# Kernel tuning notes

Measured on AMD Instinct MI355X. Metric: run time of the kernel, lower is better.

## Reference

```python
import jax, jax.numpy as jnp
import numpy as np

N = 8192      # nodes
K_NN = 32     # kNN neighbors (module default k=32)
E = N * 16    # edges for TAGConv graph
EPS = 1e-5    # BatchNorm eps


def setup_inputs() -> dict:
    key = jax.random.key(0)
    ks = iter(jax.random.split(key, 64))
    def lin(i, o):
        return jax.random.normal(next(ks), (i, o), jnp.float32) / np.float32(np.sqrt(i))
    def vec(c, scale=0.02):
        return jax.random.normal(next(ks), (c,), jnp.float32) * scale
    inp = {}
    inp["pos"] = jax.random.normal(next(ks), (N, 3), jnp.float32)
    inp["x"] = jax.random.normal(next(ks), (N, 4), jnp.float32)
    inp["edge_index"] = jax.random.randint(next(ks), (2, E), 0, N, jnp.int32)
    # conv1 edge-MLP [2*3, 64, 64, 64]
    inp["mlp1_W1"] = lin(6, 64)
    inp["mlp1_W23"] = jnp.stack([lin(64, 64), lin(64, 64)])
    inp["mlp1_b"] = jnp.stack([vec(64) for _ in range(3)])
    inp["mlp1_g"] = 1.0 + jnp.stack([vec(64) for _ in range(3)])
    inp["mlp1_beta"] = jnp.stack([vec(64) for _ in range(3)])
    # conv2 edge-MLP [2*64, 128]
    inp["mlp2_W"] = lin(128, 128); inp["mlp2_b"] = vec(128)
    inp["mlp2_g"] = 1.0 + vec(128); inp["mlp2_beta"] = vec(128)
    # lin1 MLP [128+64, 512]
    inp["lin1_W"] = lin(192, 512); inp["lin1_b"] = vec(512)
    inp["lin1_g"] = 1.0 + vec(512); inp["lin1_beta"] = vec(512)
    # TAGConv(4,64,K=3) and TAGConv(64,128,K=3): K+1 hop weights each, shared bias
    inp["tag1_W"] = jnp.stack([lin(4, 64) for _ in range(4)]); inp["tag1_b"] = vec(64)
    inp["tag2_W"] = jnp.stack([lin(64, 128) for _ in range(4)]); inp["tag2_b"] = vec(128)
    # lin_gcnn1 MLP [128+64, 512]
    inp["lin2_W"] = lin(192, 512); inp["lin2_b"] = vec(512)
    inp["lin2_g"] = 1.0 + vec(512); inp["lin2_beta"] = vec(512)
    # mix_output: MLP[1024,512] -> Dropout -> MLP[512,256] -> Dropout -> Lin(256,1)
    inp["mix1_W"] = lin(1024, 512); inp["mix1_b"] = vec(512)
    inp["mix1_g"] = 1.0 + vec(512); inp["mix1_beta"] = vec(512)
    inp["mix2_W"] = lin(512, 256); inp["mix2_b"] = vec(256)
    inp["mix2_g"] = 1.0 + vec(256); inp["mix2_beta"] = vec(256)
    inp["out_W"] = lin(256, 1); inp["out_b"] = vec(1)
    return inp


def _bn_relu_lin(h, W, b, g, beta):
    # Seq(Linear, ReLU, BatchNorm1d) with training-mode (batch) statistics
    h = jax.nn.relu(h @ W + b)
    mu = jnp.mean(h, axis=0)
    var = jnp.var(h, axis=0)
    return g * (h - mu) * jax.lax.rsqrt(var + EPS) + beta


def _knn_idx(x, k):
    # brute-force kNN (loop=False: self excluded); indices are non-differentiable
    x = jax.lax.stop_gradient(x)
    sq = jnp.sum(x * x, axis=1)
    d = sq[:, None] + sq[None, :] - 2.0 * (x @ x.T)   # [N,N] squared dists
    n = x.shape[0]
    d = d.at[jnp.arange(n), jnp.arange(n)].set(jnp.inf)
    _, idx = jax.lax.top_k(-d, k)
    return idx                                        # [N,k]


def _edge_conv(x, k, mlp_fn):
    # DynamicEdgeConv: kNN graph on x, message MLP([x_i, x_j - x_i]), max-aggregate
    idx = _knn_idx(x, k)
    xj = x[idx]                                       # [N,k,C]
    xi = jnp.broadcast_to(x[:, None, :], xj.shape)
    e = jnp.concatenate([xi, xj - xi], axis=-1).reshape(-1, 2 * x.shape[1])
    h = mlp_fn(e)                                     # [N*k, C_out]
    return jnp.max(h.reshape(x.shape[0], k, -1), axis=1)


def _tag_conv(x, W, b, row, col, norm):
    # TAGConv: out = sum_{m=0..K} (D^-1/2 A D^-1/2)^m x @ W_m + b
    out = x @ W[0]
    h = x
    for m in range(1, W.shape[0]):
        h = jax.ops.segment_sum(norm[:, None] * h[row], col, num_segments=x.shape[0])
        out = out + h @ W[m]
    return out + b


def reference(pos, x, edge_index, mlp1_W1, mlp1_W23, mlp1_b, mlp1_g, mlp1_beta,
              mlp2_W, mlp2_b, mlp2_g, mlp2_beta, lin1_W, lin1_b, lin1_g, lin1_beta,
              tag1_W, tag1_b, tag2_W, tag2_b, lin2_W, lin2_b, lin2_g, lin2_beta,
              mix1_W, mix1_b, mix1_g, mix1_beta, mix2_W, mix2_b, mix2_g, mix2_beta,
              out_W, out_b):
    def mlp1(e):
        h = _bn_relu_lin(e, mlp1_W1, mlp1_b[0], mlp1_g[0], mlp1_beta[0])
        h = _bn_relu_lin(h, mlp1_W23[0], mlp1_b[1], mlp1_g[1], mlp1_beta[1])
        return _bn_relu_lin(h, mlp1_W23[1], mlp1_b[2], mlp1_g[2], mlp1_beta[2])
    def mlp2(e):
        return _bn_relu_lin(e, mlp2_W, mlp2_b, mlp2_g, mlp2_beta)

    # --- DGCNN branch on positions ---
    x1 = _edge_conv(pos, K_NN, mlp1)                  # [N,64]
    x2 = _edge_conv(x1, K_NN, mlp2)                   # [N,128]
    out_dg = _bn_relu_lin(jnp.concatenate([x1, x2], axis=1),
                          lin1_W, lin1_b, lin1_g, lin1_beta)  # [N,512]

    # --- TAGConv branch on node features ---
    row, col = edge_index[0], edge_index[1]
    deg = jax.ops.segment_sum(jnp.ones(row.shape[0], x.dtype), col, num_segments=x.shape[0])
    dinv = jnp.where(deg > 0, jax.lax.rsqrt(jnp.maximum(deg, 1.0)), 0.0)
    norm = dinv[row] * dinv[col]
    g1 = jax.nn.relu(_tag_conv(x, tag1_W, tag1_b, row, col, norm))    # [N,64]
    g2 = jax.nn.relu(_tag_conv(g1, tag2_W, tag2_b, row, col, norm))   # [N,128]
    out_g = _bn_relu_lin(jnp.concatenate([g1, g2], axis=1),
                         lin2_W, lin2_b, lin2_g, lin2_beta)           # [N,512]

    # --- mix head (dropout = identity in eval) ---
    h = jnp.concatenate([out_dg, out_g], axis=1)      # [N,1024]
    h = _bn_relu_lin(h, mix1_W, mix1_b, mix1_g, mix1_beta)
    h = _bn_relu_lin(h, mix2_W, mix2_b, mix2_g, mix2_beta)
    return h @ out_W + out_b                          # [N,1]
```

## Files before the change

kernel.cpp:

```cpp
#include <hip/hip_runtime.h>
#include <cstdint>
#include <cstddef>

#define BN_EPS 1e-5f
#define K1CAP 1024
#define K2CAP 640

typedef short short8 __attribute__((ext_vector_type(8)));
typedef float f32x4 __attribute__((ext_vector_type(4)));
typedef unsigned long long ull;

__device__ __forceinline__ unsigned int ordf(float d) {
  unsigned int u = __float_as_uint(d);
  return (u >> 31) ? ~u : (u | 0x80000000u);
}
__device__ __forceinline__ unsigned short f2bf(float f) {
  unsigned u = __float_as_uint(f);
  u += 0x7fffu + ((u >> 16) & 1u);
  return (unsigned short)(u >> 16);
}
__device__ __forceinline__ float bf2f(unsigned short h) {
  return __uint_as_float(((unsigned)h) << 16);
}

#define BPAD 72

__global__ __launch_bounds__(256)
void mk_gemm_mfma(const float* __restrict__ A,
                  const short* __restrict__ A8h, const short* __restrict__ A8l,
                  const float* __restrict__ src, const int* __restrict__ gidx, int srcC,
                  const float* __restrict__ bnA,
                  const short* __restrict__ Wh, const short* __restrict__ Wl,
                  int ldk, int koff, int lda,
                  const float* __restrict__ bias,
                  float* __restrict__ C, short* __restrict__ Ch, short* __restrict__ Cl,
                  int ldc,
                  int M, int N, int K, int flags,
                  float* __restrict__ statsP,
                  float* __restrict__ mxp, float* __restrict__ mnp) {
  __shared__ short Ah[64][BPAD], Al[64][BPAD], Bh[64][BPAD], Bl[64][BPAD];
  __shared__ float ssum[64], ssq[64];
  int tid = threadIdx.x, lane = tid & 63, wid = tid >> 6;
  int wr = wid >> 1, wc = wid & 1;
  int r0 = blockIdx.x * 64, n0 = blockIdx.y * 64;
  int sr = tid >> 2, sc = (tid & 3) * 16;
  f32x4 zero4 = {0.f, 0.f, 0.f, 0.f};
  f32x4 acc[2][2] = {{zero4, zero4}, {zero4, zero4}};
  short8 rAh[2], rAl[2], rBh[2], rBl[2];

  auto stage = [&](int kt) {
    const short* bh = &Wh[(size_t)(n0 + sr) * ldk + koff + kt + sc];
    const short* bl = &Wl[(size_t)(n0 + sr) * ldk + koff + kt + sc];
    rBh[0] = *(const short8*)bh; rBh[1] = *(const short8*)(bh + 8);
    rBl[0] = *(const short8*)bl; rBl[1] = *(const short8*)(bl + 8);
    if (A8h) {
      const short* ah = &A8h[(size_t)(r0 + sr) * lda + kt + sc];
      const short* al = &A8l[(size_t)(r0 + sr) * lda + kt + sc];
      rAh[0] = *(const short8*)ah; rAh[1] = *(const short8*)(ah + 8);
      rAl[0] = *(const short8*)al; rAl[1] = *(const short8*)(al + 8);
    } else {
      float v[16];
      if (flags & 32) {
        int gr = r0 + sr;
        int i = gr >> 5; int j = gidx[gr];
        const float* pi = &A[(size_t)i * srcC + kt + sc];
        const float* pj = &src[(size_t)j * srcC + kt + sc];
        float va[16], vb[16];
        *(float4*)&va[0]  = *(const float4*)&pi[0];
        *(float4*)&va[4]  = *(const float4*)&pi[4];
        *(float4*)&va[8]  = *(const float4*)&pi[8];
        *(float4*)&va[12] = *(const float4*)&pi[12];
        *(float4*)&vb[0]  = *(const float4*)&pj[0];
        *(float4*)&vb[4]  = *(const float4*)&pj[4];
        *(float4*)&vb[8]  = *(const float4*)&pj[8];
        *(float4*)&vb[12] = *(const float4*)&pj[12];
#pragma unroll
        for (int e = 0; e < 16; ++e) v[e] = fmaxf(va[e] + vb[e], 0.f);
      } else {
        const float* ap = &A[(size_t)(r0 + sr) * lda + kt + sc];
        *(float4*)&v[0]  = *(const float4*)&ap[0];
        *(float4*)&v[4]  = *(const float4*)&ap[4];
        *(float4*)&v[8]  = *(const float4*)&ap[8];
        *(float4*)&v[12] = *(const float4*)&ap[12];
      }
      if (bnA) {
#pragma unroll
        for (int e = 0; e < 16; ++e) {
          int gk = kt + sc + e;
          v[e] = fmaf(bnA[gk], v[e], bnA[1024 + gk]);
        }
      }
#pragma unroll
      for (int e = 0; e < 16; ++e) {
        unsigned short h = f2bf(v[e]);
        rAh[e >> 3][e & 7] = (short)h;
        rAl[e >> 3][e & 7] = (short)f2bf(v[e] - bf2f(h));
      }
    }
  };

  stage(0);
  for (int kt = 0; kt < K; kt += 64) {
    *(short8*)&Ah[sr][sc]     = rAh[0];
    *(short8*)&Ah[sr][sc + 8] = rAh[1];
    *(short8*)&Al[sr][sc]     = rAl[0];
    *(short8*)&Al[sr][sc + 8] = rAl[1];
    *(short8*)&Bh[sr][sc]     = rBh[0];
    *(short8*)&Bh[sr][sc + 8] = rBh[1];
    *(short8*)&Bl[sr][sc]     = rBl[0];
    *(short8*)&Bl[sr][sc + 8] = rBl[1];
    __syncthreads();
    if (kt + 64 < K) stage(kt + 64);
    int ar = wr * 32 + (lane & 15);
    int br = wc * 32 + (lane & 15);
#pragma unroll
    for (int kk = 0; kk < 2; ++kk) {
      int kof = kk * 32 + (lane >> 4) * 8;
      short8 a_h[2], a_l[2], b_h[2], b_l[2];
#pragma unroll
      for (int t = 0; t < 2; ++t) {
        a_h[t] = *(const short8*)&Ah[ar + t * 16][kof];
        a_l[t] = *(const short8*)&Al[ar + t * 16][kof];
        b_h[t] = *(const short8*)&Bh[br + t * 16][kof];
        b_l[t] = *(const short8*)&Bl[br + t * 16][kof];
      }
#pragma unroll
      for (int mt = 0; mt < 2; ++mt)
#pragma unroll
        for (int nt = 0; nt < 2; ++nt) {
          acc[mt][nt] = __builtin_amdgcn_mfma_f32_16x16x32_bf16(a_h[mt], b_h[nt], acc[mt][nt], 0, 0, 0);
          acc[mt][nt] = __builtin_amdgcn_mfma_f32_16x16x32_bf16(a_h[mt], b_l[nt], acc[mt][nt], 0, 0, 0);
          acc[mt][nt] = __builtin_amdgcn_mfma_f32_16x16x32_bf16(a_l[mt], b_h[nt], acc[mt][nt], 0, 0, 0);
        }
    }
    __syncthreads();
  }
  bool dostat = (flags & 8) != 0, domx = (flags & 16) != 0;
  float lsum[2] = {0.f, 0.f}, lsq[2] = {0.f, 0.f};
  float lmx[2] = {-3.4e38f, -3.4e38f}, lmn[2] = {3.4e38f, 3.4e38f};
#pragma unroll
  for (int nt = 0; nt < 2; ++nt) {
    int gc = n0 + wc * 32 + nt * 16 + (lane & 15);
#pragma unroll
    for (int mt = 0; mt < 2; ++mt)
#pragma unroll
      for (int i = 0; i < 4; ++i) {
        int gr = r0 + wr * 32 + mt * 16 + (lane >> 4) * 4 + i;
        float v = acc[mt][nt][i];
        if (bias) v += bias[gc];
        if (flags & 1) v += C[(size_t)gr * ldc + gc];
        if (flags & 2) v = fmaxf(v, 0.f);
        if (!domx) {
          if (flags & 64) {
            unsigned short hh = f2bf(v);
            Ch[(size_t)gr * ldc + gc] = (short)hh;
            Cl[(size_t)gr * ldc + gc] = (short)f2bf(v - bf2f(hh));
          } else {
            C[(size_t)gr * ldc + gc] = v;
          }
        }
        lsum[nt] += v; lsq[nt] = fmaf(v, v, lsq[nt]);
        lmx[nt] = fmaxf(lmx[nt], v); lmn[nt] = fminf(lmn[nt], v);
      }
  }
  if (dostat || domx) {
#pragma unroll
    for (int nt = 0; nt < 2; ++nt) {
#pragma unroll
      for (int m = 16; m <= 32; m <<= 1) {
        lsum[nt] += __shfl_xor(lsum[nt], m, 64);
        lsq[nt] += __shfl_xor(lsq[nt], m, 64);
        lmx[nt] = fmaxf(lmx[nt], __shfl_xor(lmx[nt], m, 64));
        lmn[nt] = fminf(lmn[nt], __shfl_xor(lmn[nt], m, 64));
      }
    }
    if (domx && lane < 16) {
      int node = blockIdx.x * 2 + wr;
#pragma unroll
      for (int nt = 0; nt < 2; ++nt) {
        int gc = n0 + wc * 32 + nt * 16 + lane;
        mxp[(size_t)node * N + gc] = lmx[nt];
        mnp[(size_t)node * N + gc] = lmn[nt];
      }
    }
    if (dostat) {
      if (tid < 64) { ssum[tid] = 0.f; ssq[tid] = 0.f; }
      __syncthreads();
      if (lane < 16) {
#pragma unroll
        for (int nt = 0; nt < 2; ++nt) {
          int ct = wc * 32 + nt * 16 + lane;
          atomicAdd(&ssum[ct], lsum[nt]);
          atomicAdd(&ssq[ct], lsq[nt]);
        }
      }
      __syncthreads();
      if (tid < 64) {
        int slot = blockIdx.x & 63;
        int gc = n0 + tid;
        atomicAdd(&statsP[(size_t)slot * 1024 + gc], ssum[tid]);
        atomicAdd(&statsP[(size_t)slot * 1024 + 512 + gc], ssq[tid]);
      }
    }
  }
}

__global__ void mk_wcvt(const float* __restrict__ W, short* __restrict__ Wh,
                        short* __restrict__ Wl, int K, int N) {
  int g = blockIdx.x * 256 + threadIdx.x;
  if (g >= K * N) return;
  int k = g / N, n = g - k * N;
  float v = W[g];
  unsigned short h = f2bf(v);
  Wh[(size_t)n * K + k] = (short)h;
  Wl[(size_t)n * K + k] = (short)f2bf(v - bf2f(h));
}
__global__ void mk_wcvts(const float* __restrict__ W, const float* __restrict__ a,
                         short* __restrict__ Wh, short* __restrict__ Wl, int K, int N) {
  int g = blockIdx.x * 256 + threadIdx.x;
  if (g >= K * N) return;
  int k = g / N, n = g - k * N;
  float v = a[k] * W[g];
  unsigned short h = f2bf(v);
  Wh[(size_t)n * K + k] = (short)h;
  Wl[(size_t)n * K + k] = (short)f2bf(v - bf2f(h));
}
__global__ void mk_biasfold(const float* __restrict__ W, const float* __restrict__ bv,
                            const float* __restrict__ b0, float* __restrict__ bo,
                            int K, int N) {
  int col = blockIdx.x * 4 + (threadIdx.x >> 6);
  int lane = threadIdx.x & 63;
  if (col >= N) return;
  float s = 0.f;
  for (int k = lane; k < K; k += 64) s = fmaf(bv[k], W[(size_t)k * N + col], s);
#pragma unroll
  for (int off = 32; off; off >>= 1) s += __shfl_xor(s, off, 64);
  if (lane == 0) bo[col] = b0[col] + s;
}
__global__ void mk_wcvt2(const float* __restrict__ W, short* __restrict__ Dh,
                         short* __restrict__ Dl, short* __restrict__ Vh,
                         short* __restrict__ Vl) {
  int g = blockIdx.x * 256 + threadIdx.x;
  if (g >= 64 * 128) return;
  int k = g >> 7, n = g & 127;
  float u = W[k * 128 + n], vv = W[(64 + k) * 128 + n];
  float d = u - vv;
  unsigned short h = f2bf(d);
  Dh[n * 64 + k] = (short)h; Dl[n * 64 + k] = (short)f2bf(d - bf2f(h));
  h = f2bf(vv);
  Vh[n * 64 + k] = (short)h; Vl[n * 64 + k] = (short)f2bf(vv - bf2f(h));
}

__global__ void mk_conv1nodes(const float* __restrict__ pos, const float* __restrict__ W1,
                              const float* __restrict__ b1, float* __restrict__ Pp,
                              float* __restrict__ Qn) {
  int g = blockIdx.x * 256 + threadIdx.x;
  if (g >= 8192 * 64) return;
  int i = g >> 6, c = g & 63;
  float p0 = pos[i * 3], p1 = pos[i * 3 + 1], p2 = pos[i * 3 + 2];
  float q = p0 * W1[192 + c] + p1 * W1[256 + c] + p2 * W1[320 + c];
  Qn[g] = q;
  Pp[g] = p0 * W1[c] + p1 * W1[64 + c] + p2 * W1[128 + c] - q + b1[c];
}

__global__ __launch_bounds__(256)
void mk_stats1(const float* __restrict__ Pp, const float* __restrict__ Qn,
               const int* __restrict__ idx1, float* __restrict__ statsP) {
  __shared__ int sidx[512];
  int tid = threadIdx.x;
  int c = tid & 63, grp = tid >> 6;
  int nb = blockIdx.x * 16;
  if (tid < 256) {
    sidx[tid] = idx1[nb * 32 + tid];
    sidx[tid + 256] = idx1[nb * 32 + 256 + tid];
  }
  __syncthreads();
  float s = 0.f, q = 0.f;
  for (int ln = 0; ln < 16; ++ln) {
    float pv = Pp[(size_t)(nb + ln) * 64 + c];
    for (int e = grp; e < 32; e += 4) {
      int j = sidx[ln * 32 + e];
      float v = fmaxf(pv + Qn[(size_t)j * 64 + c], 0.f);
      s += v; q = fmaf(v, v, q);
    }
  }
  int slot = (blockIdx.x * 4 + grp) & 63;
  atomicAdd(&statsP[(size_t)slot * 1024 + c], s);
  atomicAdd(&statsP[(size_t)slot * 1024 + 512 + c], q);
}

__global__ __launch_bounds__(128)
void mk_econv2(const float* __restrict__ R, const float* __restrict__ T,
               const int* __restrict__ st_i, float* __restrict__ mxp,
               float* __restrict__ mnp, float* __restrict__ statsP) {
  __shared__ int sidx[256];
  int tid = threadIdx.x;
  int nb = blockIdx.x * 8;
  sidx[tid] = st_i[nb * 32 + tid];
  sidx[tid + 128] = st_i[nb * 32 + 128 + tid];
  __syncthreads();
  float s = 0.f, q = 0.f;
  for (int ln = 0; ln < 8; ++ln) {
    int i = nb + ln;
    float rv = R[(size_t)i * 128 + tid];
    float mx = -3.4e38f, mn = 3.4e38f;
    for (int e = 0; e < 32; ++e) {
      int j = sidx[ln * 32 + e];
      float v = fmaxf(rv + T[(size_t)j * 128 + tid], 0.f);
      mx = fmaxf(mx, v); mn = fminf(mn, v);
      s += v; q = fmaf(v, v, q);
    }
    mxp[(size_t)i * 128 + tid] = mx;
    mnp[(size_t)i * 128 + tid] = mn;
  }
  int slot = blockIdx.x & 63;
  atomicAdd(&statsP[(size_t)slot * 1024 + tid], s);
  atomicAdd(&statsP[(size_t)slot * 1024 + 512 + tid], q);
}

__global__ void mk_bnfinS(const float* __restrict__ sb, const float* __restrict__ g,
                          const float* __restrict__ beta, float* __restrict__ bno,
                          float Minv, int Cdim) {
  int c = blockIdx.x * 256 + threadIdx.x;
  if (c >= Cdim) return;
  float s = 0.f, q = 0.f;
  for (int sl = 0; sl < 64; ++sl) {
    s += sb[(size_t)sl * 1024 + c];
    q += sb[(size_t)sl * 1024 + 512 + c];
  }
  float mu = s * Minv;
  float var = q * Minv - mu * mu;
  float a = g[c] * rsqrtf(var + BN_EPS);
  bno[c] = a;
  bno[1024 + c] = beta[c] - a * mu;
}

__global__ void mk_finx1(const float* __restrict__ mx, const float* __restrict__ mn,
                         const float* __restrict__ bn, float* __restrict__ xc,
                         short* __restrict__ x1h, short* __restrict__ x1l) {
  int g = blockIdx.x * 256 + threadIdx.x;
  if (g >= 8192 * 64) return;
  int i = g >> 6, c = g & 63;
  float a = bn[c], b = bn[1024 + c];
  float v = (a > 0.f) ? fmaf(a, mx[g], b) : fmaf(a, mn[g], b);
  xc[(size_t)i * 192 + c] = v;
  unsigned short h = f2bf(v);
  x1h[g] = (short)h;
  x1l[g] = (short)f2bf(v - bf2f(h));
}
__global__ void mk_finx2(const float* __restrict__ mx, const float* __restrict__ mn,
                         const float* __restrict__ bn, float* __restrict__ xcB) {
  int g = blockIdx.x * 256 + threadIdx.x;
  if (g >= 8192 * 128) return;
  int i = g >> 7, c = g & 127;
  float a = bn[c], b = bn[1024 + c];
  xcB[(size_t)i * 192 + c] = (a > 0.f) ? fmaf(a, mx[g], b) : fmaf(a, mn[g], b);
}

__global__ void mk_posq(const float* __restrict__ pos, float4* __restrict__ posq) {
  int i = blockIdx.x * 256 + threadIdx.x;
  if (i >= 8192) return;
  float x = pos[i * 3], y = pos[i * 3 + 1], z = pos[i * 3 + 2];
  float s = fmaf(z, z, fmaf(y, y, x * x));
  posq[i] = make_float4(x, y, z, s);
}

__device__ __forceinline__ unsigned wave_kth8(unsigned v) {
  unsigned T = 0;
#pragma unroll
  for (int b = 31; b >= 0; --b) {
    unsigned cand = T | (1u << b);
    int c = __popcll(__ballot(v < cand));
    if (c < 8) T = cand;
  }
  return T;
}

__global__ __launch_bounds__(256)
void mk_knn1(const float4* __restrict__ posq, int* __restrict__ idxout) {
  __shared__ ull buf[K1CAP];
  __shared__ unsigned Tw[4];
  __shared__ unsigned cnt;
  int q = blockIdx.x, tid = threadIdx.x;
  int lane = tid & 63, wid = tid >> 6;
  float4 pq = posq[q];
  if (tid == 0) cnt = 0;
  unsigned key[32];
  unsigned vmin = 0xFFFFFFFFu;
#pragma unroll
  for (int c = 0; c < 32; ++c) {
    int j = c * 256 + tid;
    float4 pj = posq[j];
    float d = pq.w + pj.w - 2.f * (pq.x * pj.x + pq.y * pj.y + pq.z * pj.z);
    unsigned k = (j == q) ? 0xFFFFFFFFu : ordf(d);
    key[c] = k;
    vmin = vmin < k ? vmin : k;
  }
  unsigned T = wave_kth8(vmin);
  if (lane == 0) Tw[wid] = T;
  __syncthreads();
  unsigned Tmax = max(max(Tw[0], Tw[1]), max(Tw[2], Tw[3]));
#pragma unroll
  for (int c = 0; c < 32; ++c) {
    if (key[c] <= Tmax) {
      int j = c * 256 + tid;
      unsigned s = atomicAdd(&cnt, 1u);
      if (s < K1CAP) buf[s] = (((ull)key[c]) << 32) | (unsigned)j;
    }
  }
  __syncthreads();
  int m = cnt < (unsigned)K1CAP ? (int)cnt : K1CAP;
  for (int e = tid; e < m; e += 256) {
    ull mine = buf[e];
    int rank = 0;
    for (int f = 0; f < m; ++f) rank += (buf[f] < mine) ? 1 : 0;
    if (rank < 32) idxout[q * 32 + rank] = (int)(unsigned)(mine & 0xFFFFFFFFu);
  }
}

__global__ __launch_bounds__(256)
void mk_knn2(const float* __restrict__ S, const float* __restrict__ sq,
             int c0, int first,
             unsigned* __restrict__ st_k, int* __restrict__ st_i) {
  __shared__ ull buf[K2CAP];
  __shared__ unsigned Tw[4];
  __shared__ unsigned cnt;
  int q = blockIdx.x, tid = threadIdx.x;
  int lane = tid & 63, wid = tid >> 6;
  float sqq = sq[q];
  if (tid == 0) cnt = 0;
  unsigned key[8];
  unsigned vmin = 0xFFFFFFFFu;
#pragma unroll
  for (int c = 0; c < 8; ++c) {
    int t = c * 256 + tid;
    int j = c0 + t;
    float d = sqq + sq[j] - 2.f * S[(size_t)q * 2048 + t];
    unsigned k = (j == q) ? 0xFFFFFFFFu : ordf(d);
    key[c] = k;
    vmin = vmin < k ? vmin : k;
  }
  unsigned T = wave_kth8(vmin);
  if (lane == 0) Tw[wid] = T;
  __syncthreads();
  unsigned Tmax = max(max(Tw[0], Tw[1]), max(Tw[2], Tw[3]));
#pragma unroll
  for (int c = 0; c < 8; ++c) {
    if (key[c] <= Tmax) {
      int j = c0 + c * 256 + tid;
      unsigned s = atomicAdd(&cnt, 1u);
      if (s < K2CAP) buf[s] = (((ull)key[c]) << 32) | (unsigned)j;
    }
  }
  if (!first && tid < 32) {
    ull k = (((ull)st_k[q * 32 + tid]) << 32) | (unsigned)st_i[q * 32 + tid];
    unsigned s = atomicAdd(&cnt, 1u);
    if (s < K2CAP) buf[s] = k;
  }
  __syncthreads();
  int m = cnt < (unsigned)K2CAP ? (int)cnt : K2CAP;
  for (int e = tid; e < m; e += 256) {
    ull mine = buf[e];
    int rank = 0;
    for (int f = 0; f < m; ++f) rank += (buf[f] < mine) ? 1 : 0;
    if (rank < 32) {
      st_k[q * 32 + rank] = (unsigned)(mine >> 32);
      st_i[q * 32 + rank] = (int)(unsigned)(mine & 0xFFFFFFFFu);
    }
  }
}

#define GBM 64
#define GBN 64
#define GBK 16

__global__ __launch_bounds__(256)
void mk_gemm(const float* __restrict__ A, const float* __restrict__ W, int ldw,
             const float* __restrict__ bias, float* __restrict__ C, int ldc,
             int M, int N, int K, int flags) {
  __shared__ float As[GBK][GBM + 4];
  __shared__ float Ws[GBK][GBN];
  int tid = threadIdx.x;
  int r0 = blockIdx.x * GBM, n0 = blockIdx.y * GBN;
  int ty = tid >> 4, tx = tid & 15;
  float acc[4][4] = {};
  for (int kt = 0; kt < K; kt += GBK) {
#pragma unroll
    for (int it = 0; it < 4; ++it) {
      int l = it * 256 + tid;
      int r = l >> 4, kk = l & 15;
      int gr = r0 + r, gk = kt + kk;
      float v = 0.f;
      if (gk < K && gr < M) v = A[(size_t)gr * K + gk];
      As[kk][r] = v;
      int kw = l >> 6, nw = l & 63;
      int gkw = kt + kw;
      Ws[kw][nw] = (gkw < K && (n0 + nw) < N) ? W[(size_t)gkw * ldw + n0 + nw] : 0.f;
    }
    __syncthreads();
#pragma unroll
    for (int kk = 0; kk < GBK; ++kk) {
      float4 a4 = *(const float4*)&As[kk][ty * 4];
      float4 b4 = *(const float4*)&Ws[kk][tx * 4];
      float av[4] = {a4.x, a4.y, a4.z, a4.w};
      float bv[4] = {b4.x, b4.y, b4.z, b4.w};
#pragma unroll
      for (int i = 0; i < 4; ++i)
#pragma unroll
        for (int j = 0; j < 4; ++j)
          acc[i][j] = fmaf(av[i], bv[j], acc[i][j]);
    }
    __syncthreads();
  }
#pragma unroll
  for (int i = 0; i < 4; ++i) {
    int gr = r0 + ty * 4 + i;
    if (gr >= M) continue;
#pragma unroll
    for (int j = 0; j < 4; ++j) {
      int gc = n0 + tx * 4 + j;
      if (gc >= N) continue;
      float v = acc[i][j];
      if (bias) v += bias[gc];
      if (flags & 1) v += C[(size_t)gr * ldc + gc];
      if (flags & 2) v = fmaxf(v, 0.f);
      C[(size_t)gr * ldc + gc] = v;
    }
  }
}

__global__ void mk_sqnorm(const float* __restrict__ x, int ld, float* __restrict__ sq,
                          int Npts, int Cdim) {
  int i = blockIdx.x * blockDim.x + threadIdx.x;
  if (i >= Npts) return;
  float s = 0.f;
  for (int c = 0; c < Cdim; ++c) { float v = x[(size_t)i * ld + c]; s = fmaf(v, v, s); }
  sq[i] = s;
}

__global__ void mk_count(const int* __restrict__ col, int* __restrict__ cnt, int E) {
  int e = blockIdx.x * 256 + threadIdx.x;
  if (e < E) atomicAdd(&cnt[col[e]], 1);
}
__global__ __launch_bounds__(1024)
void mk_scan(const int* __restrict__ cnt, int* __restrict__ offp,
             int* __restrict__ cur, float* __restrict__ dinvf) {
  __shared__ int wsum[16];
  __shared__ int wexc[16];
  int t = threadIdx.x, lane = t & 63, w = t >> 6;
  int v[8]; int s = 0;
  int base = t * 8;
#pragma unroll
  for (int k = 0; k < 8; ++k) { v[k] = s; s += cnt[base + k]; }
  int sc = s;
#pragma unroll
  for (int off2 = 1; off2 < 64; off2 <<= 1) {
    int n = __shfl_up(sc, off2, 64);
    if (lane >= off2) sc += n;
  }
  if (lane == 63) wsum[w] = sc;
  __syncthreads();
  if (w == 0) {
    int x = (lane < 16) ? wsum[lane] : 0;
    int scx = x;
#pragma unroll
    for (int off2 = 1; off2 < 16; off2 <<= 1) {
      int n = __shfl_up(scx, off2, 64);
      if (lane >= off2) scx += n;
    }
    if (lane < 16) wexc[lane] = scx - x;
  }
  __syncthreads();
  int texc = wexc[w] + (sc - s);
#pragma unroll
  for (int k = 0; k < 8; ++k) {
    int o = texc + v[k];
    offp[base + k] = o;
    cur[base + k] = o;
    int d = cnt[base + k];
    dinvf[base + k] = (d > 0) ? rsqrtf((float)(d < 1 ? 1 : d)) : 0.f;
  }
  if (t == 1023) offp[8192] = texc + s;
}
__global__ void mk_fill(const int* __restrict__ row, const int* __restrict__ col,
                        const float* __restrict__ dinvf, int* __restrict__ cur,
                        int* __restrict__ crow, float* __restrict__ cw, int E) {
  int e = blockIdx.x * 256 + threadIdx.x;
  if (e >= E) return;
  int c = col[e], r = row[e];
  int s = atomicAdd(&cur[c], 1);
  crow[s] = r;
  cw[s] = dinvf[r] * dinvf[c];
}
__global__ void mk_prop64(const float* __restrict__ in, int in_ld,
                          const int* __restrict__ offp, const int* __restrict__ crow,
                          const float* __restrict__ cw, float* __restrict__ out, int out_ld) {
  int gid = blockIdx.x * 256 + threadIdx.x;
  if (gid >= 8192 * 16) return;
  int col = gid >> 4, c4 = (gid & 15) * 4;
  int s0 = offp[col], s1 = offp[col + 1];
  float a0 = 0, a1 = 0, a2 = 0, a3 = 0;
  for (int s = s0; s < s1; ++s) {
    int r = crow[s]; float w = cw[s];
    float4 v = *(const float4*)&in[(size_t)r * in_ld + c4];
    a0 = fmaf(w, v.x, a0); a1 = fmaf(w, v.y, a1);
    a2 = fmaf(w, v.z, a2); a3 = fmaf(w, v.w, a3);
  }
  float4 o = {a0, a1, a2, a3};
  *(float4*)&out[(size_t)col * out_ld + c4] = o;
}
__global__ void mk_prop4(const float* __restrict__ in, int in_ld,
                         const int* __restrict__ offp, const int* __restrict__ crow,
                         const float* __restrict__ cw, float* __restrict__ out, int out_ld) {
  int col = blockIdx.x * 256 + threadIdx.x;
  if (col >= 8192) return;
  int s0 = offp[col], s1 = offp[col + 1];
  float a0 = 0, a1 = 0, a2 = 0, a3 = 0;
  for (int s = s0; s < s1; ++s) {
    int r = crow[s]; float w = cw[s];
    float4 v = *(const float4*)&in[(size_t)r * in_ld];
    a0 = fmaf(w, v.x, a0); a1 = fmaf(w, v.y, a1);
    a2 = fmaf(w, v.z, a2); a3 = fmaf(w, v.w, a3);
  }
  float4 o = {a0, a1, a2, a3};
  *(float4*)&out[(size_t)col * out_ld] = o;
}
__global__ void mk_pack4(const float* __restrict__ xin, float* __restrict__ H1) {
  int g = blockIdx.x * 256 + threadIdx.x;
  if (g >= 8192 * 4) return;
  H1[(size_t)(g >> 2) * 16 + (g & 3)] = xin[g];
}
__global__ void mk_copy64(const float* __restrict__ gcv, float* __restrict__ H2) {
  int g = blockIdx.x * 256 + threadIdx.x;
  if (g >= 8192 * 64) return;
  H2[(size_t)(g >> 6) * 256 + (g & 63)] = gcv[(size_t)(g >> 6) * 192 + (g & 63)];
}

__global__ __launch_bounds__(256)
void mk_gemv_out(const float* __restrict__ h, const float* __restrict__ bn,
                 const float* __restrict__ w, const float* __restrict__ b,
                 float* __restrict__ out, int Npts) {
  int row = blockIdx.x * 4 + (threadIdx.x >> 6);
  int lane = threadIdx.x & 63;
  if (row >= Npts) return;
  int c = lane * 4;
  float4 v = *(const float4*)&h[(size_t)row * 256 + c];
  float s = (bn[c] * v.x + bn[1024 + c]) * w[c]
          + (bn[c + 1] * v.y + bn[1024 + c + 1]) * w[c + 1]
          + (bn[c + 2] * v.z + bn[1024 + c + 2]) * w[c + 2]
          + (bn[c + 3] * v.w + bn[1024 + c + 3]) * w[c + 3];
#pragma unroll
  for (int off = 32; off; off >>= 1) s += __shfl_xor(s, off, 64);
  if (lane == 0) out[row] = s + b[0];
}

extern "C" void kernel_launch(void* const* d_in, const int* in_sizes, int n_in,
                              void* d_out, int out_size, void* d_ws, size_t ws_size,
                              hipStream_t stream) {
  const int N = 8192;
  const int NE = N * 32;
  const float* pos = (const float*)d_in[0];
  const float* xin = (const float*)d_in[1];
  const int* ei = (const int*)d_in[2];
  const int E = in_sizes[2] / 2;
  const int* erow = ei;
  const int* ecol = ei + E;
  const float* mlp1_W1  = (const float*)d_in[3];
  const float* mlp1_W23 = (const float*)d_in[4];
  const float* mlp1_b   = (const float*)d_in[5];
  const float* mlp1_g   = (const float*)d_in[6];
  const float* mlp1_be  = (const float*)d_in[7];
  const float* mlp2_W   = (const float*)d_in[8];
  const float* mlp2_b   = (const float*)d_in[9];
  const float* mlp2_g   = (const float*)d_in[10];
  const float* mlp2_be  = (const float*)d_in[11];
  const float* lin1_W   = (const float*)d_in[12];
  const float* lin1_b   = (const float*)d_in[13];
  const float* lin1_g   = (const float*)d_in[14];
  const float* lin1_be  = (const float*)d_in[15];
  const float* tag1_W   = (const float*)d_in[16];
  const float* tag1_b   = (const float*)d_in[17];
  const float* tag2_W   = (const float*)d_in[18];
  const float* tag2_b   = (const float*)d_in[19];
  const float* lin2_W   = (const float*)d_in[20];
  const float* lin2_b   = (const float*)d_in[21];
  const float* lin2_g   = (const float*)d_in[22];
  const float* lin2_be  = (const float*)d_in[23];
  const float* mix1_W   = (const float*)d_in[24];
  const float* mix1_b   = (const float*)d_in[25];
  const float* mix1_g   = (const float*)d_in[26];
  const float* mix1_be  = (const float*)d_in[27];
  const float* mix2_W   = (const float*)d_in[28];
  const float* mix2_b   = (const float*)d_in[29];
  const float* mix2_g   = (const float*)d_in[30];
  const float* mix2_be  = (const float*)d_in[31];
  const float* outW     = (const float*)d_in[32];
  const float* outB     = (const float*)d_in[33];

  char* base = (char*)d_ws;
  size_t off = 0;
  auto alloc = [&](size_t b) -> void* {
    void* p = base + off;
    off += (b + 255) & ~(size_t)255;
    return p;
  };
  float* BIG = (float*)alloc(134217728ull);
  short* h2_h  = (short*)BIG;
  short* h2_l  = (short*)((char*)BIG + 33554432);
  float* Sb    = BIG;
  short* mhcat_h = (short*)BIG;
  short* mhcat_l = (short*)((char*)BIG + 16777216);
  short* mh1_h   = (short*)((char*)BIG + 33554432);
  short* mh1_l   = (short*)((char*)BIG + 41943040);
  float* mh2     = (float*)((char*)BIG + 50331648);
  float* H2      = BIG + 16777216;
  int*   idx1 = (int*)alloc((size_t)NE * 4);
  unsigned* st_k = (unsigned*)alloc((size_t)NE * 4);
  int*   st_i = (int*)alloc((size_t)NE * 4);
  float* xc  = (float*)alloc((size_t)N * 192 * 4);
  float* gc  = (float*)alloc((size_t)N * 192 * 4);
  float4* posq = (float4*)alloc((size_t)N * 16);
  float* sqx = (float*)alloc((size_t)N * 4);
  float* Pp  = (float*)alloc((size_t)N * 64 * 4);
  float* Qn  = (float*)alloc((size_t)N * 64 * 4);
  float* Rb  = (float*)alloc((size_t)N * 128 * 4);
  float* Tb  = (float*)alloc((size_t)N * 128 * 4);
  float* mx1 = (float*)alloc((size_t)N * 64 * 4);
  float* mn1 = (float*)alloc((size_t)N * 64 * 4);
  float* mx2 = (float*)alloc((size_t)N * 128 * 4);
  float* mn2 = (float*)alloc((size_t)N * 128 * 4);
  float* H1  = (float*)alloc((size_t)N * 16 * 4);
  float* dinvf = (float*)alloc((size_t)N * 4);
  int* cnt     = (int*)alloc((size_t)N * 4);
  int* csr_off = (int*)alloc((size_t)(N + 1) * 4);
  int* cursor  = (int*)alloc((size_t)N * 4);
  int* csr_row = (int*)alloc((size_t)E * 4);
  float* csr_w = (float*)alloc((size_t)E * 4);
  float* slotAll = (float*)alloc((size_t)8 * 64 * 1024 * 4);
  auto slot = [&](int i) { return slotAll + (size_t)i * 64 * 1024; };
  float* bnb = (float*)alloc(8 * 2048 * 4);
  auto bnp = [&](int i) { return bnb + (size_t)i * 2048; };
  float* bnM = bnp(4);
  float* bias1f = (float*)alloc(512 * 4);
  float* bias2f = (float*)alloc(256 * 4);
  float* biasA  = (float*)alloc(64 * 4);
  float* biasB  = (float*)alloc(64 * 4);
  auto salloc = [&](size_t n) { return (short*)alloc(n * 2); };
  short* w23a_h = salloc(4096);   short* w23a_l = salloc(4096);
  short* w23b_h = salloc(4096);   short* w23b_l = salloc(4096);
  short* wd2_h  = salloc(8192);   short* wd2_l  = salloc(8192);
  short* wv2_h  = salloc(8192);   short* wv2_l  = salloc(8192);
  short* wl1_h  = salloc(98304);  short* wl1_l  = salloc(98304);
  short* wt2_h  = salloc(32768);  short* wt2_l  = salloc(32768);
  short* wl2_h  = salloc(98304);  short* wl2_l  = salloc(98304);
  short* wx1_h  = salloc(524288); short* wx1_l  = salloc(524288);
  short* wx2_h  = salloc(131072); short* wx2_l  = salloc(131072);
  short* x1h    = salloc(524288); short* x1l    = salloc(524288);

  auto gemmF = [&](const float* A, const short* A8h, const short* A8l,
                   const float* src, const int* gidx, int srcC, const float* bnA,
                   const short* Wh_, const short* Wl_, int ldk, int koff, int lda,
                   const float* bias, float* Cp, short* Chp, short* Clp, int ldc,
                   int M, int Nn, int Kk, int flags,
                   float* stP = nullptr, float* mxP = nullptr, float* mnP = nullptr) {
    dim3 g(M / 64, Nn / 64);
    mk_gemm_mfma<<<g, 256, 0, stream>>>(A, A8h, A8l, src, gidx, srcC, bnA,
                                        Wh_, Wl_, ldk, koff, lda, bias, Cp, Chp, Clp, ldc,
                                        M, Nn, Kk, flags, stP, mxP, mnP);
  };
  auto wcvt = [&](const float* W, short* Wh_, short* Wl_, int Kk, int Nn) {
    mk_wcvt<<<(Kk * Nn + 255) / 256, 256, 0, stream>>>(W, Wh_, Wl_, Kk, Nn);
  };

  hipMemsetAsync(slotAll, 0, (size_t)8 * 64 * 1024 * 4, stream);
  hipMemsetAsync(cnt, 0, (size_t)N * 4, stream);
  mk_wcvt2<<<(64 * 128 + 255) / 256, 256, 0, stream>>>(mlp2_W, wd2_h, wd2_l, wv2_h, wv2_l);
  wcvt(lin1_W, wl1_h, wl1_l, 192, 512);
  wcvt(tag2_W, wt2_h, wt2_l, 256, 128);
  wcvt(lin2_W, wl2_h, wl2_l, 192, 512);

  mk_posq<<<32, 256, 0, stream>>>(pos, posq);
  mk_knn1<<<N, 256, 0, stream>>>(posq, idx1);

  mk_conv1nodes<<<(N * 64 + 255) / 256, 256, 0, stream>>>(pos, mlp1_W1, mlp1_b, Pp, Qn);
  mk_stats1<<<512, 256, 0, stream>>>(Pp, Qn, idx1, slot(0));
  mk_bnfinS<<<1, 256, 0, stream>>>(slot(0), mlp1_g, mlp1_be, bnp(0), 1.f / NE, 64);
  mk_wcvts<<<(64 * 64 + 255) / 256, 256, 0, stream>>>(mlp1_W23, bnp(0), w23a_h, w23a_l, 64, 64);
  mk_biasfold<<<16, 256, 0, stream>>>(mlp1_W23, bnp(0) + 1024, mlp1_b + 64, biasA, 64, 64);
  gemmF(Pp, nullptr, nullptr, Qn, idx1, 64, nullptr,
        w23a_h, w23a_l, 64, 0, 64, biasA, nullptr, h2_h, h2_l, 64,
        NE, 64, 64, 2 | 8 | 32 | 64, slot(1));
  mk_bnfinS<<<1, 256, 0, stream>>>(slot(1), mlp1_g + 64, mlp1_be + 64, bnp(1), 1.f / NE, 64);
  mk_wcvts<<<(64 * 64 + 255) / 256, 256, 0, stream>>>(mlp1_W23 + 4096, bnp(1), w23b_h, w23b_l, 64, 64);
  mk_biasfold<<<16, 256, 0, stream>>>(mlp1_W23 + 4096, bnp(1) + 1024, mlp1_b + 128, biasB, 64, 64);
  gemmF(nullptr, h2_h, h2_l, nullptr, nullptr, 0, nullptr,
        w23b_h, w23b_l, 64, 0, 64, biasB, nullptr, nullptr, nullptr, 64,
        NE, 64, 64, 2 | 8 | 16, slot(2), mx1, mn1);
  mk_bnfinS<<<1, 256, 0, stream>>>(slot(2), mlp1_g + 128, mlp1_be + 128, bnp(2), 1.f / NE, 64);
  mk_finx1<<<(N * 64 + 255) / 256, 256, 0, stream>>>(mx1, mn1, bnp(2), xc, x1h, x1l);

  mk_sqnorm<<<32, 256, 0, stream>>>(xc, 192, sqx, N, 64);
  for (int c = 0; c < 4; ++c) {
    gemmF(nullptr, x1h, x1l, nullptr, nullptr, 0, nullptr,
          x1h + (size_t)c * 2048 * 64, x1l + (size_t)c * 2048 * 64, 64, 0, 64,
          nullptr, Sb, nullptr, nullptr, 2048, N, 2048, 64, 0);
    mk_knn2<<<N, 256, 0, stream>>>(Sb, sqx, c * 2048, c == 0 ? 1 : 0, st_k, st_i);
  }

  gemmF(nullptr, x1h, x1l, nullptr, nullptr, 0, nullptr,
        wd2_h, wd2_l, 64, 0, 64, mlp2_b, Rb, nullptr, nullptr, 128, N, 128, 64, 0);
  gemmF(nullptr, x1h, x1l, nullptr, nullptr, 0, nullptr,
        wv2_h, wv2_l, 64, 0, 64, nullptr, Tb, nullptr, nullptr, 128, N, 128, 64, 0);
  mk_econv2<<<N / 8, 128, 0, stream>>>(Rb, Tb, st_i, mx2, mn2, slot(3));
  mk_bnfinS<<<1, 256, 0, stream>>>(slot(3), mlp2_g, mlp2_be, bnp(3), 1.f / NE, 128);
  mk_finx2<<<(N * 128 + 255) / 256, 256, 0, stream>>>(mx2, mn2, bnp(3), xc + 64);

  gemmF(xc, nullptr, nullptr, nullptr, nullptr, 0, nullptr,
        wl1_h, wl1_l, 192, 0, 192, lin1_b, nullptr, mhcat_h, mhcat_l, 1024,
        N, 512, 192, 2 | 8 | 64, slot(4));
  mk_bnfinS<<<2, 256, 0, stream>>>(slot(4), lin1_g, lin1_be, bnM, 1.f / N, 512);

  mk_count<<<(E + 255) / 256, 256, 0, stream>>>(ecol, cnt, E);
  mk_scan<<<1, 1024, 0, stream>>>(cnt, csr_off, cursor, dinvf);
  mk_fill<<<(E + 255) / 256, 256, 0, stream>>>(erow, ecol, dinvf, cursor, csr_row, csr_w, E);
  mk_pack4<<<(N * 4 + 255) / 256, 256, 0, stream>>>(xin, H1);
  mk_prop4<<<32, 256, 0, stream>>>(xin, 4, csr_off, csr_row, csr_w, H1 + 4, 16);
  mk_prop4<<<32, 256, 0, stream>>>(H1 + 4, 16, csr_off, csr_row, csr_w, H1 + 8, 16);
  mk_prop4<<<32, 256, 0, stream>>>(H1 + 8, 16, csr_off, csr_row, csr_w, H1 + 12, 16);
  mk_gemm<<<dim3(128, 1), 256, 0, stream>>>(H1, tag1_W, 64, tag1_b, gc, 192, N, 64, 16, 2);
  mk_copy64<<<(N * 64 + 255) / 256, 256, 0, stream>>>(gc, H2);
  mk_prop64<<<512, 256, 0, stream>>>(gc, 192, csr_off, csr_row, csr_w, H2 + 64, 256);
  mk_prop64<<<512, 256, 0, stream>>>(H2 + 64, 256, csr_off, csr_row, csr_w, H2 + 128, 256);
  mk_prop64<<<512, 256, 0, stream>>>(H2 + 128, 256, csr_off, csr_row, csr_w, H2 + 192, 256);
  gemmF(H2, nullptr, nullptr, nullptr, nullptr, 0, nullptr,
        wt2_h, wt2_l, 256, 0, 256, tag2_b, gc + 64, nullptr, nullptr, 192,
        N, 128, 256, 2);
  gemmF(gc, nullptr, nullptr, nullptr, nullptr, 0, nullptr,
        wl2_h, wl2_l, 192, 0, 192, lin2_b, nullptr, mhcat_h + 512, mhcat_l + 512, 1024,
        N, 512, 192, 2 | 8 | 64, slot(5));
  mk_bnfinS<<<2, 256, 0, stream>>>(slot(5), lin2_g, lin2_be, bnM + 512, 1.f / N, 512);

  mk_wcvts<<<(1024 * 512 + 255) / 256, 256, 0, stream>>>(mix1_W, bnM, wx1_h, wx1_l, 1024, 512);
  mk_biasfold<<<128, 256, 0, stream>>>(mix1_W, bnM + 1024, mix1_b, bias1f, 1024, 512);
  gemmF(nullptr, mhcat_h, mhcat_l, nullptr, nullptr, 0, nullptr,
        wx1_h, wx1_l, 1024, 0, 1024, bias1f, nullptr, mh1_h, mh1_l, 512,
        N, 512, 1024, 2 | 8 | 64, slot(6));
  mk_bnfinS<<<2, 256, 0, stream>>>(slot(6), mix1_g, mix1_be, bnp(6), 1.f / N, 512);
  mk_wcvts<<<(512 * 256 + 255) / 256, 256, 0, stream>>>(mix2_W, bnp(6), wx2_h, wx2_l, 512, 256);
  mk_biasfold<<<64, 256, 0, stream>>>(mix2_W, bnp(6) + 1024, mix2_b, bias2f, 512, 256);
  gemmF(nullptr, mh1_h, mh1_l, nullptr, nullptr, 0, nullptr,
        wx2_h, wx2_l, 512, 0, 512, bias2f, mh2, nullptr, nullptr, 256,
        N, 256, 512, 2 | 8, slot(7));
  mk_bnfinS<<<1, 256, 0, stream>>>(slot(7), mix2_g, mix2_be, bnp(7), 1.f / N, 256);
  mk_gemv_out<<<N / 4, 256, 0, stream>>>(mh2, bnp(7), outW, outB, (float*)d_out, N);
}
```

Measured before the change: 714.1 us.

## Fuse kNN distance key computation into GEMM epilogue and enlarge chunks

The GEMM epilogue gains a flag that turns the inner products directly into ordered distance keys using the squared norms, writing unsigned keys instead of floats. mk_knn2 now just loads precomputed keys, and the candidate loop covers 4096 columns in 2 chunks instead of 2048 in 4, which halves launches and merge passes. In mk_knn1 the self-exclusion moves from key computation to insertion, with the threshold raised to the 9th smallest to compensate. Costs are more registers per thread in knn2 and epilogue work in the GEMM.

```diff
diff --git a/kernel.cpp b/kernel.cpp
--- a/kernel.cpp
+++ b/kernel.cpp
@@ -151,7 +151,12 @@
         if (flags & 1) v += C[(size_t)gr * ldc + gc];
         if (flags & 2) v = fmaxf(v, 0.f);
         if (!domx) {
-          if (flags & 64) {
+          if (flags & 128) {
+            int gj = srcC + gc;
+            unsigned kk2 = (gr == gj) ? 0xFFFFFFFFu
+                                      : ordf(src[gr] + src[gj] - 2.f * v);
+            ((unsigned*)C)[(size_t)gr * ldc + gc] = kk2;
+          } else if (flags & 64) {
             unsigned short hh = f2bf(v);
             Ch[(size_t)gr * ldc + gc] = (short)hh;
             Cl[(size_t)gr * ldc + gc] = (short)f2bf(v - bf2f(hh));
@@ -365,13 +370,13 @@
   posq[i] = make_float4(x, y, z, s);
 }
 
-__device__ __forceinline__ unsigned wave_kth8(unsigned v) {
+__device__ __forceinline__ unsigned wave_kth(unsigned v, int kk) {
   unsigned T = 0;
 #pragma unroll
   for (int b = 31; b >= 0; --b) {
     unsigned cand = T | (1u << b);
     int c = __popcll(__ballot(v < cand));
-    if (c < 8) T = cand;
+    if (c < kk) T = cand;
   }
   return T;
 }
@@ -392,11 +397,11 @@
     int j = c * 256 + tid;
     float4 pj = posq[j];
     float d = pq.w + pj.w - 2.f * (pq.x * pj.x + pq.y * pj.y + pq.z * pj.z);
-    unsigned k = (j == q) ? 0xFFFFFFFFu : ordf(d);
+    unsigned k = ordf(d);
     key[c] = k;
     vmin = vmin < k ? vmin : k;
   }
-  unsigned T = wave_kth8(vmin);
+  unsigned T = wave_kth(vmin, 9);
   if (lane == 0) Tw[wid] = T;
   __syncthreads();
   unsigned Tmax = max(max(Tw[0], Tw[1]), max(Tw[2], Tw[3]));
@@ -404,8 +409,10 @@
   for (int c = 0; c < 32; ++c) {
     if (key[c] <= Tmax) {
       int j = c * 256 + tid;
-      unsigned s = atomicAdd(&cnt, 1u);
-      if (s < K1CAP) buf[s] = (((ull)key[c]) << 32) | (unsigned)j;
+      if (j != q) {
+        unsigned s = atomicAdd(&cnt, 1u);
+        if (s < K1CAP) buf[s] = (((ull)key[c]) << 32) | (unsigned)j;
+      }
     }
   }
   __syncthreads();
@@ -419,33 +426,28 @@
 }
 
 __global__ __launch_bounds__(256)
-void mk_knn2(const float* __restrict__ S, const float* __restrict__ sq,
-             int c0, int first,
+void mk_knn2(const unsigned* __restrict__ Kb, int c0, int first,
              unsigned* __restrict__ st_k, int* __restrict__ st_i) {
   __shared__ ull buf[K2CAP];
   __shared__ unsigned Tw[4];
   __shared__ unsigned cnt;
   int q = blockIdx.x, tid = threadIdx.x;
   int lane = tid & 63, wid = tid >> 6;
-  float sqq = sq[q];
   if (tid == 0) cnt = 0;
-  unsigned key[8];
+  unsigned key[16];
   unsigned vmin = 0xFFFFFFFFu;
 #pragma unroll
-  for (int c = 0; c < 8; ++c) {
-    int t = c * 256 + tid;
-    int j = c0 + t;
-    float d = sqq + sq[j] - 2.f * S[(size_t)q * 2048 + t];
-    unsigned k = (j == q) ? 0xFFFFFFFFu : ordf(d);
+  for (int c = 0; c < 16; ++c) {
+    unsigned k = Kb[(size_t)q * 4096 + c * 256 + tid];
     key[c] = k;
     vmin = vmin < k ? vmin : k;
   }
-  unsigned T = wave_kth8(vmin);
+  unsigned T = wave_kth(vmin, 8);
   if (lane == 0) Tw[wid] = T;
   __syncthreads();
   unsigned Tmax = max(max(Tw[0], Tw[1]), max(Tw[2], Tw[3]));
 #pragma unroll
-  for (int c = 0; c < 8; ++c) {
+  for (int c = 0; c < 16; ++c) {
     if (key[c] <= Tmax) {
       int j = c0 + c * 256 + tid;
       unsigned s = atomicAdd(&cnt, 1u);
@@ -707,7 +709,7 @@
   float* BIG = (float*)alloc(134217728ull);
   short* h2_h  = (short*)BIG;
   short* h2_l  = (short*)((char*)BIG + 33554432);
-  float* Sb    = BIG;
+  unsigned* Kb = (unsigned*)BIG;
   short* mhcat_h = (short*)BIG;
   short* mhcat_l = (short*)((char*)BIG + 16777216);
   short* mh1_h   = (short*)((char*)BIG + 33554432);
@@ -800,11 +802,11 @@
   mk_finx1<<<(N * 64 + 255) / 256, 256, 0, stream>>>(mx1, mn1, bnp(2), xc, x1h, x1l);
 
   mk_sqnorm<<<32, 256, 0, stream>>>(xc, 192, sqx, N, 64);
-  for (int c = 0; c < 4; ++c) {
-    gemmF(nullptr, x1h, x1l, nullptr, nullptr, 0, nullptr,
-          x1h + (size_t)c * 2048 * 64, x1l + (size_t)c * 2048 * 64, 64, 0, 64,
-          nullptr, Sb, nullptr, nullptr, 2048, N, 2048, 64, 0);
-    mk_knn2<<<N, 256, 0, stream>>>(Sb, sqx, c * 2048, c == 0 ? 1 : 0, st_k, st_i);
+  for (int c = 0; c < 2; ++c) {
+    gemmF(nullptr, x1h, x1l, sqx, nullptr, c * 4096, nullptr,
+          x1h + (size_t)c * 4096 * 64, x1l + (size_t)c * 4096 * 64, 64, 0, 64,
+          nullptr, (float*)Kb, nullptr, nullptr, 4096, N, 4096, 64, 128);
+    mk_knn2<<<N, 256, 0, stream>>>(Kb, c * 4096, c == 0 ? 1 : 0, st_k, st_i);
   }
 
   gemmF(nullptr, x1h, x1l, nullptr, nullptr, 0, nullptr,
```

New measurement: 699.2 us. 1.02x faster.
